# Kernel optimization log

Hardware: AMD Instinct MI355X
Metric: run time of the kernel (lower is better)

Reference implementation:

```python
import jax, jax.numpy as jnp
import numpy as np
from jax import lax

N, C, RC, H, W = 2, 256, 32, 64, 64  # RC = C // 8


def conv1x1(x, w, b):
    # x: [n,c,h,w], w: [o,c], b: [o]
    return jnp.einsum('nchw,oc->nohw', x, w) + b[None, :, None, None]


def conv3x3(x, w, b):
    # x: [n,c,h,w], w: [o,i,3,3]
    y = lax.conv_general_dilated(x, w, window_strides=(1, 1), padding='SAME',
                                 dimension_numbers=('NCHW', 'OIHW', 'NCHW'))
    return y + b[None, :, None, None]


def setup_inputs() -> dict:
    key = jax.random.key(0)
    ks = jax.random.split(key, 16)
    p = lambda k, s: jax.random.normal(k, s, dtype=jnp.float32) * 0.02
    z = lambda o: jnp.zeros((o,), jnp.float32)
    return {
        'rgb_feat': jax.random.normal(ks[0], (N, C, H, W), jnp.float32),
        'chm_feat': jax.random.normal(ks[1], (N, C, H, W), jnp.float32),
        'rgb_q_w': p(ks[2], (RC, C)), 'rgb_q_b': z(RC),
        'rgb_k_w': p(ks[3], (RC, C)), 'rgb_k_b': z(RC),
        'rgb_v_w': p(ks[4], (C, C)), 'rgb_v_b': z(C),
        'depth_q_w': p(ks[5], (RC, C)), 'depth_q_b': z(RC),
        'depth_k_w': p(ks[6], (RC, C)), 'depth_k_b': z(RC),
        'depth_v_w': p(ks[7], (C, C)), 'depth_v_b': z(C),
        'gate_w': p(ks[8], (C, 2 * C)), 'gate_b': z(C),
        'fus1_w': p(ks[9], (2 * C, 2 * C)), 'fus1_b': z(2 * C),
        'fus2_w': p(ks[10], (2 * C, 2 * C, 3, 3)), 'fus2_b': z(2 * C),
        'fus3_w': p(ks[11], (C, 2 * C)), 'fus3_b': z(C),
        'skip_w': p(ks[12], (C, 2 * C)), 'skip_b': z(C),
    }


def reference(rgb_feat, chm_feat,
              rgb_q_w, rgb_q_b, rgb_k_w, rgb_k_b, rgb_v_w, rgb_v_b,
              depth_q_w, depth_q_b, depth_k_w, depth_k_b, depth_v_w, depth_v_b,
              gate_w, gate_b, fus1_w, fus1_b, fus2_w, fus2_b,
              fus3_w, fus3_b, skip_w, skip_b):
    n, c, h, w = rgb_feat.shape
    hw = h * w
    flat = lambda t: t.reshape(n, t.shape[1], hw)

    rq = flat(conv1x1(rgb_feat, rgb_q_w, rgb_q_b))       # [n,rc,hw]
    rk = flat(conv1x1(rgb_feat, rgb_k_w, rgb_k_b))       # [n,rc,hw]
    rv = flat(conv1x1(rgb_feat, rgb_v_w, rgb_v_b))       # [n,c,hw]
    dq = flat(conv1x1(chm_feat, depth_q_w, depth_q_b))   # [n,rc,hw]
    dk = flat(conv1x1(chm_feat, depth_k_w, depth_k_b))   # [n,rc,hw]
    dv = flat(conv1x1(chm_feat, depth_v_w, depth_v_b))   # [n,c,hw]

    # rgb branch attended with depth-derived attention
    rgb_attn = jax.nn.softmax(jnp.einsum('nri,nrj->nij', dq, dk), axis=-1)  # [n,hw,hw]
    br = jnp.einsum('nci,nij->ncj', rv, rgb_attn).reshape(rgb_feat.shape) + rgb_feat

    # depth branch attended with rgb-derived attention
    depth_attn = jax.nn.softmax(jnp.einsum('nri,nrj->nij', rq, rk), axis=-1)
    bd = jnp.einsum('nci,nij->ncj', dv, depth_attn).reshape(chm_feat.shape) + chm_feat

    cat = jnp.concatenate([br, bd], axis=1)              # [n,2c,h,w]
    g = jax.nn.sigmoid(conv1x1(cat, gate_w, gate_b))     # [n,c,h,w]
    c_fused = br * g + bd * (1.0 - g)
    d_fused = br * bd
    f = jnp.concatenate([c_fused, d_fused], axis=1)      # [n,2c,h,w]

    y = jax.nn.relu(conv1x1(f, fus1_w, fus1_b))
    y = jax.nn.relu(conv3x3(y, fus2_w, fus2_b))
    y = conv1x1(y, fus3_w, fus3_b)
    fused = y + conv1x1(f, skip_w, skip_b)
    return fused
```

## Files before the change

### kernel.cpp

```cpp
#include <hip/hip_runtime.h>
#include <stdint.h>


typedef __bf16 bf16_t;
typedef __bf16 bf16x8 __attribute__((ext_vector_type(8)));
typedef float f32x4 __attribute__((ext_vector_type(4)));

#define HW 4096
#define NB 2

__device__ inline f32x4 mfma_bf16(bf16x8 a, bf16x8 b, f32x4 c) {
    return __builtin_amdgcn_mfma_f32_16x16x32_bf16(a, b, c, 0, 0, 0);
}

#define MAXJOB 12
struct CvtJobs {
    const float* src[MAXJOB];
    bf16_t* dst[MAXJOB];
    int vend[MAXJOB];
    int rowlen[MAXJOB];
    int rowstride[MAXJOB];
    int rowoff[MAXJOB];
};

__global__ __launch_bounds__(256) void convert_batch_k(CvtJobs J, int totalvec) {
    int gv = blockIdx.x * 256 + threadIdx.x;
    if (gv >= totalvec) return;
    int j = 0;
    while (gv >= J.vend[j]) j++;
    int vbase = (j == 0) ? 0 : J.vend[j - 1];
    int e = (gv - vbase) * 8;
    const float* s = J.src[j] + e;
    float4 f0 = *(const float4*)s;
    float4 f1 = *(const float4*)(s + 4);
    bf16x8 o;
    o[0] = (bf16_t)f0.x; o[1] = (bf16_t)f0.y; o[2] = (bf16_t)f0.z; o[3] = (bf16_t)f0.w;
    o[4] = (bf16_t)f1.x; o[5] = (bf16_t)f1.y; o[6] = (bf16_t)f1.z; o[7] = (bf16_t)f1.w;
    int di = e;
    if (J.rowlen[j])
        di = (e / J.rowlen[j]) * J.rowstride[j] + J.rowoff[j] + (e % J.rowlen[j]);
    *(bf16x8*)(J.dst[j] + di) = o;
}

__global__ __launch_bounds__(256) void pack_bias_k(const float* qr, const float* kr,
                                                   const float* qd, const float* kd,
                                                   const float* sb, const float* fb,
                                                   float* BQK_R, float* BQK_D, float* BSUM) {
    int t = threadIdx.x;
    if (t < 32) {
        BQK_R[t] = qr[t]; BQK_R[32 + t] = kr[t];
        BQK_D[t] = qd[t]; BQK_D[32 + t] = kd[t];
    }
    BSUM[t] = sb[t] + fb[t];
}

__global__ __launch_bounds__(256) void reorder_fus2_k(const float* __restrict__ src,
                                                      bf16_t* __restrict__ dst) {
    int idx = blockIdx.x * 256 + threadIdx.x;
    if (idx >= 512 * 4608) return;
    int o = idx / 4608;
    int t = idx % 4608;
    int t9 = t / 512;
    int c  = t % 512;
    dst[idx] = (bf16_t)src[(size_t)o * 4608 + c * 9 + t9];
}

template <int EPI, bool OUT_BF16, int NW>
__global__ __launch_bounds__(NW * 64) void gemm_k(const bf16_t* __restrict__ A,
                                                  const bf16_t* __restrict__ A2,
                                                  const bf16_t* __restrict__ B,
                                                  const float* __restrict__ bias,
                                                  const float* __restrict__ bias2,
                                                  void* __restrict__ outp,
                                                  const void* __restrict__ aux,
                                                  int M, int K, size_t strideB, size_t strideO) {
    __shared__ bf16_t Bt[64][72];
    const int t = threadIdx.x;
    const int mb = blockIdx.x, jb = blockIdx.y, n = blockIdx.z;
    const int w = t >> 6, lane = t & 63, quad = lane >> 4, l16 = lane & 15;
    const int MBLK = NW * 16;

    const bf16_t* Au = (n >= 2) ? A2 : A;
    const float* biasu = (n >= 2) ? bias2 : bias;

    const bf16_t* Bb = B + (size_t)n * strideB + jb * 64;

    f32x4 zero = {0.f, 0.f, 0.f, 0.f};
    f32x4 acc[4] = {zero, zero, zero, zero};

    const bf16_t* Arow = Au + (size_t)(mb * MBLK + w * 16 + l16) * K + quad * 8;

    for (int k0 = 0; k0 < K; k0 += 64) {
        if constexpr (NW == 4) {
            const bf16_t* src = Bb + (size_t)(k0 + lane) * HW + w * 16;
            bf16x8 v0 = *(const bf16x8*)src;
            bf16x8 v1 = *(const bf16x8*)(src + 8);
            __syncthreads();
#pragma unroll
            for (int e = 0; e < 8; e++) Bt[w * 16 + e][lane] = v0[e];
#pragma unroll
            for (int e = 0; e < 8; e++) Bt[w * 16 + 8 + e][lane] = v1[e];
        } else {
            const bf16_t* src = Bb + (size_t)(k0 + lane) * HW + w * 8;
            bf16x8 v0 = *(const bf16x8*)src;
            __syncthreads();
#pragma unroll
            for (int e = 0; e < 8; e++) Bt[w * 8 + e][lane] = v0[e];
        }
        __syncthreads();

        bf16x8 a0 = *(const bf16x8*)(Arow + k0);
        bf16x8 a1 = *(const bf16x8*)(Arow + k0 + 32);
#pragma unroll
        for (int ns = 0; ns < 4; ns++) {
            bf16x8 b0 = *(const bf16x8*)&Bt[ns * 16 + l16][quad * 8];
            bf16x8 b1 = *(const bf16x8*)&Bt[ns * 16 + l16][32 + quad * 8];
            acc[ns] = mfma_bf16(a0, b0, acc[ns]);
            acc[ns] = mfma_bf16(a1, b1, acc[ns]);
        }
    }

    if (EPI == 6) {
        const float scl = (w < 2) ? 1.44269504f : 1.0f;
#pragma unroll
        for (int ns = 0; ns < 4; ns++) {
            int col = jb * 64 + ns * 16 + l16;
            union { bf16_t h[4]; unsigned long long u; } pk;
#pragma unroll
            for (int rr = 0; rr < 4; rr++) {
                int m = w * 16 + quad * 4 + rr;
                pk.h[rr] = (bf16_t)((acc[ns][rr] + biasu[m]) * scl);
            }
            *(unsigned long long*)((bf16_t*)outp +
                ((size_t)n * HW + col) * 64 + w * 16 + quad * 4) = pk.u;
        }
    } else if (EPI == 7) {
        const int m_base = mb * MBLK + w * 16 + quad * 4;
#pragma unroll
        for (int ns = 0; ns < 4; ns++) {
            int col = jb * 64 + ns * 16 + l16;
            union { bf16_t h[4]; unsigned long long u; } pk;
#pragma unroll
            for (int rr = 0; rr < 4; rr++) {
                float v = acc[ns][rr] + biasu[m_base + rr];
                pk.h[rr] = (bf16_t)(v > 0.f ? v : 0.f);
            }
            *(unsigned long long*)((bf16_t*)outp +
                ((size_t)n * HW + col) * 512 + m_base) = pk.u;
        }
    } else if (EPI == 5) {
        const bf16_t* catp = (const bf16_t*)aux;
        bf16_t* f = (bf16_t*)outp;
#pragma unroll
        for (int ns = 0; ns < 4; ns++) {
#pragma unroll
            for (int rr = 0; rr < 4; rr++) {
                int m = mb * MBLK + w * 16 + quad * 4 + rr;
                int col = jb * 64 + ns * 16 + l16;
                float v = acc[ns][rr] + biasu[m];
                float g = 1.f / (1.f + __expf(-v));
                size_t base = (size_t)n * 512 * HW + (size_t)m * HW + col;
                float br = (float)catp[base];
                float bd = (float)catp[base + (size_t)256 * HW];
                size_t ob = (size_t)n * 1024 * HW + (size_t)m * HW + col;
                f[ob] = (bf16_t)(br * g + bd * (1.f - g));
                f[ob + (size_t)256 * HW] = (bf16_t)(br * bd);
            }
        }
    } else {
#pragma unroll
        for (int ns = 0; ns < 4; ns++) {
#pragma unroll
            for (int rr = 0; rr < 4; rr++) {
                int m = mb * MBLK + w * 16 + quad * 4 + rr;
                int col = jb * 64 + ns * 16 + l16;
                float v = acc[ns][rr] + biasu[m];
                if (EPI == 1) v = v > 0.f ? v : 0.f;
                size_t oi = (size_t)n * strideO + (size_t)m * HW + col;
                if (OUT_BF16) ((bf16_t*)outp)[oi] = (bf16_t)v;
                else ((float*)outp)[oi] = v;
            }
        }
    }
}

__global__ __launch_bounds__(256) void conv3_k(const bf16_t* __restrict__ A,
                                               const bf16_t* __restrict__ Y1n,
                                               const float* __restrict__ bias,
                                               bf16_t* __restrict__ outp,
                                               size_t strideN) {
    __shared__ bf16_t kTn[198][72];
    const int t = threadIdx.x;
    const int lin = blockIdx.x;
    const int n = lin & 1, mb = (lin >> 1) & 3, y = lin >> 3;
    const int w = t >> 6, lane = t & 63, quad = lane >> 4, l16 = lane & 15;

    f32x4 zero = {0.f, 0.f, 0.f, 0.f};
    f32x4 acc[2][4];
#pragma unroll
    for (int i = 0; i < 2; i++)
#pragma unroll
        for (int j = 0; j < 4; j++) acc[i][j] = zero;

    const bf16_t* Yb = Y1n + (size_t)n * HW * 512;

    const bf16_t* Arow0 = A + (size_t)(mb * 128 + w * 32 + l16) * 4608 + quad * 8;
    const bf16_t* Arow1 = Arow0 + (size_t)16 * 4608;

    int pxs[7], seg[7], gidx[7];
    bool ok[7], act[7];
#pragma unroll
    for (int i = 0; i < 7; i++) {
        int slot = t + i * 256;
        act[i] = slot < 1584;
        int ps = act[i] ? (slot >> 3) : 0;
        pxs[i] = ps;
        seg[i] = slot & 7;
        int r = ps / 66, xm = ps % 66;
        int yy = y + r - 1, xx = xm - 1;
        ok[i] = act[i] && ((unsigned)yy < 64u) && ((unsigned)xx < 64u);
        gidx[i] = ok[i] ? (yy * 64 + xx) : 0;
    }

    for (int c0 = 0; c0 < 512; c0 += 64) {
        bf16x8 vals[7];
#pragma unroll
        for (int i = 0; i < 7; i++) {
            bf16x8 v;
            if (ok[i]) {
                v = *(const bf16x8*)(Yb + (size_t)gidx[i] * 512 + c0 + seg[i] * 8);
            } else {
#pragma unroll
                for (int e = 0; e < 8; e++) v[e] = (bf16_t)0.f;
            }
            vals[i] = v;
        }
        __syncthreads();
#pragma unroll
        for (int i = 0; i < 7; i++)
            if (act[i]) *(bf16x8*)&kTn[pxs[i]][seg[i] * 8] = vals[i];
        __syncthreads();

#pragma unroll
        for (int t9 = 0; t9 < 9; t9++) {
            const int dy = t9 / 3, dx = t9 % 3;
            const bf16_t* ap0 = Arow0 + t9 * 512 + c0;
            const bf16_t* ap1 = Arow1 + t9 * 512 + c0;
            bf16x8 a00 = *(const bf16x8*)(ap0);
            bf16x8 a01 = *(const bf16x8*)(ap0 + 32);
            bf16x8 a10 = *(const bf16x8*)(ap1);
            bf16x8 a11 = *(const bf16x8*)(ap1 + 32);
#pragma unroll
            for (int ns = 0; ns < 4; ns++) {
                int p = dy * 66 + ns * 16 + l16 + dx;
                bf16x8 b0 = *(const bf16x8*)&kTn[p][quad * 8];
                bf16x8 b1 = *(const bf16x8*)&kTn[p][32 + quad * 8];
                acc[0][ns] = mfma_bf16(a00, b0, acc[0][ns]);
                acc[0][ns] = mfma_bf16(a01, b1, acc[0][ns]);
                acc[1][ns] = mfma_bf16(a10, b0, acc[1][ns]);
                acc[1][ns] = mfma_bf16(a11, b1, acc[1][ns]);
            }
        }
    }

#pragma unroll
    for (int ms = 0; ms < 2; ms++) {
#pragma unroll
        for (int ns = 0; ns < 4; ns++) {
#pragma unroll
            for (int rr = 0; rr < 4; rr++) {
                int m = mb * 128 + w * 32 + ms * 16 + quad * 4 + rr;
                int x = ns * 16 + l16;
                float v = acc[ms][ns][rr] + bias[m];
                v = v > 0.f ? v : 0.f;
                outp[(size_t)n * strideN + (size_t)m * HW + y * 64 + x] = (bf16_t)v;
            }
        }
    }
}

#define ASTEP(P, ASC, AVC, ASN, AVN, ITN)                                      \
    {                                                                          \
        _Pragma("unroll")                                                      \
        for (int ns = 0; ns < 4; ns++) {                                       \
            f32x4 s = mfma_bf16(ASC, bS[ns], zero);                            \
            union { bf16_t h[4]; unsigned long long u; } pk;                   \
            float zs = 0.f;                                                    \
            _Pragma("unroll")                                                  \
            for (int rr = 0; rr < 4; rr++) {                                   \
                pk.h[rr] = (bf16_t)__builtin_amdgcn_exp2f(s[rr]);              \
                zs += (float)pk.h[rr];                                         \
            }                                                                  \
            zacc[ns] += zs;                                                    \
            *(unsigned long long*)&PT[P][ns * 16 + l16][w * 16 + quad * 4] = pk.u; \
        }                                                                      \
        ASN = *(const bf16x8*)(Qa + (size_t)((ITN) & 63) * (64 * 64));         \
        AVN[0][0] = *(const bf16x8*)(Vr0 + ((ITN) & 63) * 64);                 \
        AVN[0][1] = *(const bf16x8*)(Vr0 + ((ITN) & 63) * 64 + 32);            \
        AVN[1][0] = *(const bf16x8*)(Vr1 + ((ITN) & 63) * 64);                 \
        AVN[1][1] = *(const bf16x8*)(Vr1 + ((ITN) & 63) * 64 + 32);            \
        asm volatile("s_waitcnt lgkmcnt(0)" ::: "memory");                     \
        __builtin_amdgcn_s_barrier();                                          \
        __builtin_amdgcn_sched_barrier(0);                                     \
        __builtin_amdgcn_s_setprio(1);                                         \
        _Pragma("unroll")                                                      \
        for (int ns = 0; ns < 4; ns++) {                                       \
            bf16x8 b0 = *(const bf16x8*)&PT[P][ns * 16 + l16][quad * 8];       \
            bf16x8 b1 = *(const bf16x8*)&PT[P][ns * 16 + l16][32 + quad * 8];  \
            _Pragma("unroll")                                                  \
            for (int ct = 0; ct < 2; ct++) {                                   \
                acc[ct][ns] = mfma_bf16(AVC[ct][0], b0, acc[ct][ns]);          \
                acc[ct][ns] = mfma_bf16(AVC[ct][1], b1, acc[ct][ns]);          \
            }                                                                  \
        }                                                                      \
        __builtin_amdgcn_s_setprio(0);                                         \
    }

__global__ __launch_bounds__(256) void attn3_k(const bf16_t* __restrict__ QKT,
                                               const bf16_t* __restrict__ V,
                                               const float* __restrict__ rgb_feat,
                                               const float* __restrict__ chm_feat,
                                               bf16_t* __restrict__ CAT) {
    __shared__ bf16_t PT[2][64][72];
    __shared__ float Zp[4][64];
    const int t = threadIdx.x;
    const int lin = blockIdx.x;
    const int cb = lin & 1, z = (lin >> 1) & 3, jb = lin >> 3;
    const int w = t >> 6, lane = t & 63, quad = lane >> 4, l16 = lane & 15;
    const int qs = z ^ 2, n = z & 1;

    const bf16_t* Q = QKT + (size_t)qs * HW * 64;

    bf16x8 bS[4];
#pragma unroll
    for (int ns = 0; ns < 4; ns++)
        bS[ns] = *(const bf16x8*)(Q + (size_t)(jb * 64 + ns * 16 + l16) * 64 + 32 + quad * 8);

    f32x4 zero = {0.f, 0.f, 0.f, 0.f};
    f32x4 acc[2][4];
#pragma unroll
    for (int i = 0; i < 2; i++)
#pragma unroll
        for (int j = 0; j < 4; j++) acc[i][j] = zero;
    float zacc[4] = {0.f, 0.f, 0.f, 0.f};

    const bf16_t* Vr0 = V + ((size_t)z * 256 + cb * 128 + w * 16 + l16) * HW + quad * 8;
    const bf16_t* Vr1 = Vr0 + (size_t)64 * HW;
    const bf16_t* Qa = Q + (size_t)(w * 16 + l16) * 64 + quad * 8;

    bf16x8 aSa, aSb, aVa[2][2], aVb[2][2];
    aSa = *(const bf16x8*)Qa;
    aVa[0][0] = *(const bf16x8*)(Vr0);
    aVa[0][1] = *(const bf16x8*)(Vr0 + 32);
    aVa[1][0] = *(const bf16x8*)(Vr1);
    aVa[1][1] = *(const bf16x8*)(Vr1 + 32);

    for (int ii = 0; ii < 32; ii++) {
        ASTEP(0, aSa, aVa, aSb, aVb, 2 * ii + 1);
        ASTEP(1, aSb, aVb, aSa, aVa, 2 * ii + 2);
    }

#pragma unroll
    for (int ns = 0; ns < 4; ns++) {
        zacc[ns] += __shfl_xor(zacc[ns], 16, 64);
        zacc[ns] += __shfl_xor(zacc[ns], 32, 64);
    }
    if (lane < 16) {
#pragma unroll
        for (int ns = 0; ns < 4; ns++) Zp[w][ns * 16 + lane] = zacc[ns];
    }
    __syncthreads();
    float rz[4];
#pragma unroll
    for (int ns = 0; ns < 4; ns++) {
        float ssum = 0.f;
#pragma unroll
        for (int ww = 0; ww < 4; ww++) ssum += Zp[ww][ns * 16 + l16];
        rz[ns] = 1.f / ssum;
    }

    const float* feat = ((z < 2) ? rgb_feat : chm_feat) + (size_t)n * 256 * HW;
    bf16_t* outp = CAT + (size_t)n * 512 * HW + (size_t)(z < 2 ? 0 : 256) * HW;
#pragma unroll
    for (int ct = 0; ct < 2; ct++) {
#pragma unroll
        for (int ns = 0; ns < 4; ns++) {
#pragma unroll
            for (int rr = 0; rr < 4; rr++) {
                int c = cb * 128 + ct * 64 + w * 16 + quad * 4 + rr;
                int col = jb * 64 + ns * 16 + l16;
                float v = acc[ct][ns][rr] * rz[ns] + feat[(size_t)c * HW + col];
                outp[(size_t)c * HW + col] = (bf16_t)v;
            }
        }
    }
}

extern "C" void kernel_launch(void* const* d_in, const int* in_sizes, int n_in,
                              void* d_out, int out_size, void* d_ws, size_t ws_size,
                              hipStream_t stream) {
    (void)in_sizes; (void)n_in; (void)out_size; (void)ws_size;

    const float* rgb_feat  = (const float*)d_in[0];
    const float* chm_feat  = (const float*)d_in[1];
    const float* rgb_q_w   = (const float*)d_in[2];
    const float* rgb_q_b   = (const float*)d_in[3];
    const float* rgb_k_w   = (const float*)d_in[4];
    const float* rgb_k_b   = (const float*)d_in[5];
    const float* rgb_v_w   = (const float*)d_in[6];
    const float* rgb_v_b   = (const float*)d_in[7];
    const float* depth_q_w = (const float*)d_in[8];
    const float* depth_q_b = (const float*)d_in[9];
    const float* depth_k_w = (const float*)d_in[10];
    const float* depth_k_b = (const float*)d_in[11];
    const float* depth_v_w = (const float*)d_in[12];
    const float* depth_v_b = (const float*)d_in[13];
    const float* gate_w    = (const float*)d_in[14];
    const float* gate_b    = (const float*)d_in[15];
    const float* fus1_w    = (const float*)d_in[16];
    const float* fus1_b    = (const float*)d_in[17];
    const float* fus2_w    = (const float*)d_in[18];
    const float* fus2_b    = (const float*)d_in[19];
    const float* fus3_w    = (const float*)d_in[20];
    const float* fus3_b    = (const float*)d_in[21];
    const float* skip_w    = (const float*)d_in[22];
    const float* skip_b    = (const float*)d_in[23];

    char* ws = (char*)d_ws;
    size_t off = 0;
    auto alloc = [&](size_t bytes) -> char* {
        char* p = ws + off;
        off += (bytes + 255) & ~(size_t)255;
        return p;
    };

    bf16_t* WQK_R = (bf16_t*)alloc(64 * 256 * 2);
    bf16_t* WQK_D = (bf16_t*)alloc(64 * 256 * 2);
    bf16_t* WV_R  = (bf16_t*)alloc(256 * 256 * 2);
    bf16_t* WV_D  = (bf16_t*)alloc(256 * 256 * 2);
    bf16_t* WGATE = (bf16_t*)alloc(256 * 512 * 2);
    bf16_t* WFUS1 = (bf16_t*)alloc(512 * 512 * 2);
    bf16_t* WFUS2 = (bf16_t*)alloc(512 * 4608 * 2);
    bf16_t* WCAT  = (bf16_t*)alloc(256 * 1024 * 2);
    float*  BQK_R = (float*)alloc(64 * 4);
    float*  BQK_D = (float*)alloc(64 * 4);
    float*  BSUM  = (float*)alloc(256 * 4);
    bf16_t* XB    = (bf16_t*)alloc((size_t)4 * 256 * HW * 2);
    bf16_t* QKT   = (bf16_t*)alloc((size_t)4 * HW * 64 * 2);
    bf16_t* V4    = (bf16_t*)alloc((size_t)4 * 256 * HW * 2);
    bf16_t* CAT   = (bf16_t*)alloc((size_t)NB * 512 * HW * 2);
    bf16_t* FY    = (bf16_t*)alloc((size_t)NB * 1024 * HW * 2);
    bf16_t* Y1    = (bf16_t*)alloc((size_t)NB * HW * 512 * 2);

    bf16_t* XR = XB;
    bf16_t* XC = XB + (size_t)2 * 256 * HW;

    CvtJobs J;
    int cum = 0, nj = 0;
    auto addjob = [&](const float* s, bf16_t* d, int cnt, int rl, int rs, int ro) {
        J.src[nj] = s; J.dst[nj] = d; cum += cnt / 8; J.vend[nj] = cum;
        J.rowlen[nj] = rl; J.rowstride[nj] = rs; J.rowoff[nj] = ro; nj++;
    };
    addjob(rgb_feat, XR, NB * 256 * HW, 0, 0, 0);
    addjob(chm_feat, XC, NB * 256 * HW, 0, 0, 0);
    addjob(rgb_q_w, WQK_R, 32 * 256, 0, 0, 0);
    addjob(rgb_k_w, WQK_R + 32 * 256, 32 * 256, 0, 0, 0);
    addjob(depth_q_w, WQK_D, 32 * 256, 0, 0, 0);
    addjob(depth_k_w, WQK_D + 32 * 256, 32 * 256, 0, 0, 0);
    addjob(rgb_v_w, WV_R, 256 * 256, 0, 0, 0);
    addjob(depth_v_w, WV_D, 256 * 256, 0, 0, 0);
    addjob(gate_w, WGATE, 256 * 512, 0, 0, 0);
    addjob(fus1_w, WFUS1, 512 * 512, 0, 0, 0);
    addjob(skip_w, WCAT, 256 * 512, 512, 1024, 0);
    addjob(fus3_w, WCAT, 256 * 512, 512, 1024, 512);
    int totalvec = cum;
    convert_batch_k<<<dim3((totalvec + 255) / 256), 256, 0, stream>>>(J, totalvec);
    reorder_fus2_k<<<dim3(512 * 4608 / 256), 256, 0, stream>>>(fus2_w, WFUS2);
    pack_bias_k<<<dim3(1), 256, 0, stream>>>(rgb_q_b, rgb_k_b, depth_q_b, depth_k_b,
                                             skip_b, fus3_b, BQK_R, BQK_D, BSUM);

    gemm_k<6, true, 4><<<dim3(1, 64, 4), 256, 0, stream>>>(
        WQK_R, WQK_D, XB, BQK_R, BQK_D, QKT, nullptr, 64, 256, (size_t)256 * HW, 0);

    gemm_k<0, true, 8><<<dim3(2, 64, 4), 512, 0, stream>>>(
        WV_R, WV_D, XB, rgb_v_b, depth_v_b, V4, nullptr, 256, 256, (size_t)256 * HW, (size_t)256 * HW);

    attn3_k<<<dim3(512), 256, 0, stream>>>(QKT, V4, rgb_feat, chm_feat, CAT);

    gemm_k<5, true, 8><<<dim3(2, 64, NB), 512, 0, stream>>>(
        WGATE, WGATE, CAT, gate_b, gate_b, FY, CAT, 256, 512, (size_t)512 * HW, 0);

    gemm_k<7, true, 8><<<dim3(4, 64, NB), 512, 0, stream>>>(
        WFUS1, WFUS1, FY, fus1_b, fus1_b, Y1, nullptr, 512, 512, (size_t)1024 * HW, 0);

    conv3_k<<<dim3(512), 256, 0, stream>>>(WFUS2, Y1, fus2_b,
                                           FY + (size_t)512 * HW, (size_t)1024 * HW);

    gemm_k<0, false, 8><<<dim3(2, 64, NB), 512, 0, stream>>>(
        WCAT, WCAT, FY, BSUM, BSUM, d_out, nullptr, 256, 1024, (size_t)1024 * HW, (size_t)256 * HW);
}
```

Before: 339.2 us.

## Merge prep kernels, fuse QK and V projections, prefetch global tiles across barriers

Folds the three setup kernels (convert, fus2 reorder, bias pack) into one launch, and merges the QK and V projection GEMMs into a single kernel with 640 blocks. The GEMM and conv3 main loops now issue the next K-chunk's global load before the MFMAs and store it to LDS after the barrier, which is software prefetching. A custom barrier waits only on LDS counters so those in-flight global loads are not drained. This cuts launch overhead and hides load latency, at the cost of extra registers and a wasted wrap-around prefetch on the last iteration.

```diff
diff --git a/kernel.cpp b/kernel.cpp
--- a/kernel.cpp
+++ b/kernel.cpp
@@ -12,6 +12,13 @@
 __device__ inline f32x4 mfma_bf16(bf16x8 a, bf16x8 b, f32x4 c) {
     return __builtin_amdgcn_mfma_f32_16x16x32_bf16(a, b, c, 0, 0, 0);
 }
+
+#define LBAR()                                                                 \
+    do {                                                                       \
+        asm volatile("s_waitcnt lgkmcnt(0)" ::: "memory");                     \
+        __builtin_amdgcn_s_barrier();                                          \
+        __builtin_amdgcn_sched_barrier(0);                                     \
+    } while (0)
 
 #define MAXJOB 12
 struct CvtJobs {
@@ -23,62 +30,163 @@
     int rowoff[MAXJOB];
 };
 
-__global__ __launch_bounds__(256) void convert_batch_k(CvtJobs J, int totalvec) {
-    int gv = blockIdx.x * 256 + threadIdx.x;
-    if (gv >= totalvec) return;
-    int j = 0;
-    while (gv >= J.vend[j]) j++;
-    int vbase = (j == 0) ? 0 : J.vend[j - 1];
-    int e = (gv - vbase) * 8;
-    const float* s = J.src[j] + e;
-    float4 f0 = *(const float4*)s;
-    float4 f1 = *(const float4*)(s + 4);
-    bf16x8 o;
-    o[0] = (bf16_t)f0.x; o[1] = (bf16_t)f0.y; o[2] = (bf16_t)f0.z; o[3] = (bf16_t)f0.w;
-    o[4] = (bf16_t)f1.x; o[5] = (bf16_t)f1.y; o[6] = (bf16_t)f1.z; o[7] = (bf16_t)f1.w;
-    int di = e;
-    if (J.rowlen[j])
-        di = (e / J.rowlen[j]) * J.rowstride[j] + J.rowoff[j] + (e % J.rowlen[j]);
-    *(bf16x8*)(J.dst[j] + di) = o;
-}
-
-__global__ __launch_bounds__(256) void pack_bias_k(const float* qr, const float* kr,
-                                                   const float* qd, const float* kd,
-                                                   const float* sb, const float* fb,
-                                                   float* BQK_R, float* BQK_D, float* BSUM) {
-    int t = threadIdx.x;
-    if (t < 32) {
-        BQK_R[t] = qr[t]; BQK_R[32 + t] = kr[t];
-        BQK_D[t] = qd[t]; BQK_D[32 + t] = kd[t];
-    }
-    BSUM[t] = sb[t] + fb[t];
-}
-
-__global__ __launch_bounds__(256) void reorder_fus2_k(const float* __restrict__ src,
-                                                      bf16_t* __restrict__ dst) {
-    int idx = blockIdx.x * 256 + threadIdx.x;
-    if (idx >= 512 * 4608) return;
-    int o = idx / 4608;
-    int t = idx % 4608;
-    int t9 = t / 512;
-    int c  = t % 512;
-    dst[idx] = (bf16_t)src[(size_t)o * 4608 + c * 9 + t9];
-}
-
-template <int EPI, bool OUT_BF16, int NW>
-__global__ __launch_bounds__(NW * 64) void gemm_k(const bf16_t* __restrict__ A,
-                                                  const bf16_t* __restrict__ A2,
-                                                  const bf16_t* __restrict__ B,
-                                                  const float* __restrict__ bias,
-                                                  const float* __restrict__ bias2,
-                                                  void* __restrict__ outp,
-                                                  const void* __restrict__ aux,
-                                                  int M, int K, size_t strideB, size_t strideO) {
+__global__ __launch_bounds__(256) void prep_k(CvtJobs J, int totalvec, int cvtBlocks,
+                                              const float* __restrict__ fus2_src,
+                                              bf16_t* __restrict__ fus2_dst,
+                                              const float* qr, const float* kr,
+                                              const float* qd, const float* kd,
+                                              const float* sb, const float* fb,
+                                              float* BQK_R, float* BQK_D, float* BSUM) {
+    const int b = blockIdx.x, t = threadIdx.x;
+    if (b < cvtBlocks) {
+        int gv = b * 256 + t;
+        if (gv >= totalvec) return;
+        int j = 0;
+        while (gv >= J.vend[j]) j++;
+        int vbase = (j == 0) ? 0 : J.vend[j - 1];
+        int e = (gv - vbase) * 8;
+        const float* s = J.src[j] + e;
+        float4 f0 = *(const float4*)s;
+        float4 f1 = *(const float4*)(s + 4);
+        bf16x8 o;
+        o[0] = (bf16_t)f0.x; o[1] = (bf16_t)f0.y; o[2] = (bf16_t)f0.z; o[3] = (bf16_t)f0.w;
+        o[4] = (bf16_t)f1.x; o[5] = (bf16_t)f1.y; o[6] = (bf16_t)f1.z; o[7] = (bf16_t)f1.w;
+        int di = e;
+        if (J.rowlen[j])
+            di = (e / J.rowlen[j]) * J.rowstride[j] + J.rowoff[j] + (e % J.rowlen[j]);
+        *(bf16x8*)(J.dst[j] + di) = o;
+    } else if (b < cvtBlocks + 9216) {
+        int idx = (b - cvtBlocks) * 256 + t;
+        int o = idx / 4608;
+        int tt = idx % 4608;
+        int t9 = tt / 512;
+        int c  = tt % 512;
+        fus2_dst[idx] = (bf16_t)fus2_src[(size_t)o * 4608 + c * 9 + t9];
+    } else {
+        if (t < 32) {
+            BQK_R[t] = qr[t]; BQK_R[32 + t] = kr[t];
+            BQK_D[t] = qd[t]; BQK_D[32 + t] = kd[t];
+        }
+        BSUM[t] = sb[t] + fb[t];
+    }
+}
+
+__global__ __launch_bounds__(512) void proj_k(const bf16_t* __restrict__ WV_R,
+                                              const bf16_t* __restrict__ WV_D,
+                                              const bf16_t* __restrict__ WQK_R,
+                                              const bf16_t* __restrict__ WQK_D,
+                                              const bf16_t* __restrict__ XB,
+                                              const float* __restrict__ vb_r,
+                                              const float* __restrict__ vb_d,
+                                              const float* __restrict__ bqk_r,
+                                              const float* __restrict__ bqk_d,
+                                              bf16_t* __restrict__ V4,
+                                              bf16_t* __restrict__ QKT) {
+    __shared__ bf16_t Bt[2][64][72];
+    const int t = threadIdx.x, b = blockIdx.x;
+    const int w = t >> 6, lane = t & 63, quad = lane >> 4, l16 = lane & 15;
+
+    f32x4 zero = {0.f, 0.f, 0.f, 0.f};
+    f32x4 acc[4] = {zero, zero, zero, zero};
+
+    if (b < 512) {
+        const int mb = b & 1, jb = (b >> 1) & 63, n = b >> 7;
+        const bf16_t* Au = (n >= 2) ? WV_D : WV_R;
+        const float* biasu = (n >= 2) ? vb_d : vb_r;
+        const bf16_t* Bb = XB + (size_t)n * (256 * HW) + jb * 64;
+        const bf16_t* Arow = Au + (size_t)(mb * 128 + w * 16 + l16) * 256 + quad * 8;
+
+        bf16x8 v0 = *(const bf16x8*)(Bb + (size_t)lane * HW + w * 8);
+        for (int k0 = 0; k0 < 256; k0 += 64) {
+            LBAR();
+#pragma unroll
+            for (int e = 0; e < 8; e++) Bt[0][w * 8 + e][lane] = v0[e];
+            LBAR();
+            const int kn = (k0 + 64 < 256) ? k0 + 64 : 0;
+            bf16x8 vp = *(const bf16x8*)(Bb + (size_t)(kn + lane) * HW + w * 8);
+            bf16x8 a0 = *(const bf16x8*)(Arow + k0);
+            bf16x8 a1 = *(const bf16x8*)(Arow + k0 + 32);
+#pragma unroll
+            for (int ns = 0; ns < 4; ns++) {
+                bf16x8 b0 = *(const bf16x8*)&Bt[0][ns * 16 + l16][quad * 8];
+                bf16x8 b1 = *(const bf16x8*)&Bt[0][ns * 16 + l16][32 + quad * 8];
+                acc[ns] = mfma_bf16(a0, b0, acc[ns]);
+                acc[ns] = mfma_bf16(a1, b1, acc[ns]);
+            }
+            v0 = vp;
+        }
+#pragma unroll
+        for (int ns = 0; ns < 4; ns++) {
+#pragma unroll
+            for (int rr = 0; rr < 4; rr++) {
+                int m = mb * 128 + w * 16 + quad * 4 + rr;
+                int col = jb * 64 + ns * 16 + l16;
+                V4[(size_t)n * 256 * HW + (size_t)m * HW + col] =
+                    (bf16_t)(acc[ns][rr] + biasu[m]);
+            }
+        }
+    } else {
+        const int qb = b - 512;
+        const int n2 = qb >> 5, jpair = qb & 31;
+        const int g = w >> 2, wg = w & 3;
+        const int jb = jpair * 2 + g;
+        const bf16_t* Au = (n2 >= 2) ? WQK_D : WQK_R;
+        const float* biasu = (n2 >= 2) ? bqk_d : bqk_r;
+        const bf16_t* Bb = XB + (size_t)n2 * (256 * HW) + jb * 64;
+        const bf16_t* Arow = Au + (size_t)(wg * 16 + l16) * 256 + quad * 8;
+
+        bf16x8 v0 = *(const bf16x8*)(Bb + (size_t)lane * HW + wg * 16);
+        bf16x8 v1 = *(const bf16x8*)(Bb + (size_t)lane * HW + wg * 16 + 8);
+        for (int k0 = 0; k0 < 256; k0 += 64) {
+            LBAR();
+#pragma unroll
+            for (int e = 0; e < 8; e++) Bt[g][wg * 16 + e][lane] = v0[e];
+#pragma unroll
+            for (int e = 0; e < 8; e++) Bt[g][wg * 16 + 8 + e][lane] = v1[e];
+            LBAR();
+            const int kn = (k0 + 64 < 256) ? k0 + 64 : 0;
+            bf16x8 p0 = *(const bf16x8*)(Bb + (size_t)(kn + lane) * HW + wg * 16);
+            bf16x8 p1 = *(const bf16x8*)(Bb + (size_t)(kn + lane) * HW + wg * 16 + 8);
+            bf16x8 a0 = *(const bf16x8*)(Arow + k0);
+            bf16x8 a1 = *(const bf16x8*)(Arow + k0 + 32);
+#pragma unroll
+            for (int ns = 0; ns < 4; ns++) {
+                bf16x8 b0 = *(const bf16x8*)&Bt[g][ns * 16 + l16][quad * 8];
+                bf16x8 b1 = *(const bf16x8*)&Bt[g][ns * 16 + l16][32 + quad * 8];
+                acc[ns] = mfma_bf16(a0, b0, acc[ns]);
+                acc[ns] = mfma_bf16(a1, b1, acc[ns]);
+            }
+            v0 = p0; v1 = p1;
+        }
+        const float scl = (wg < 2) ? 1.44269504f : 1.0f;
+#pragma unroll
+        for (int ns = 0; ns < 4; ns++) {
+            int col = jb * 64 + ns * 16 + l16;
+            union { bf16_t h[4]; unsigned long long u; } pk;
+#pragma unroll
+            for (int rr = 0; rr < 4; rr++) {
+                int m = wg * 16 + quad * 4 + rr;
+                pk.h[rr] = (bf16_t)((acc[ns][rr] + biasu[m]) * scl);
+            }
+            *(unsigned long long*)(QKT +
+                ((size_t)n2 * HW + col) * 64 + wg * 16 + quad * 4) = pk.u;
+        }
+    }
+}
+
+template <int EPI, bool OUT_BF16>
+__global__ __launch_bounds__(512) void gemm_k(const bf16_t* __restrict__ A,
+                                              const bf16_t* __restrict__ A2,
+                                              const bf16_t* __restrict__ B,
+                                              const float* __restrict__ bias,
+                                              const float* __restrict__ bias2,
+                                              void* __restrict__ outp,
+                                              const void* __restrict__ aux,
+                                              int M, int K, size_t strideB, size_t strideO) {
     __shared__ bf16_t Bt[64][72];
     const int t = threadIdx.x;
     const int mb = blockIdx.x, jb = blockIdx.y, n = blockIdx.z;
     const int w = t >> 6, lane = t & 63, quad = lane >> 4, l16 = lane & 15;
-    const int MBLK = NW * 16;
 
     const bf16_t* Au = (n >= 2) ? A2 : A;
     const float* biasu = (n >= 2) ? bias2 : bias;
@@ -88,27 +196,16 @@
     f32x4 zero = {0.f, 0.f, 0.f, 0.f};
     f32x4 acc[4] = {zero, zero, zero, zero};
 
-    const bf16_t* Arow = Au + (size_t)(mb * MBLK + w * 16 + l16) * K + quad * 8;
-
+    const bf16_t* Arow = Au + (size_t)(mb * 128 + w * 16 + l16) * K + quad * 8;
+
+    bf16x8 v0 = *(const bf16x8*)(Bb + (size_t)lane * HW + w * 8);
     for (int k0 = 0; k0 < K; k0 += 64) {
-        if constexpr (NW == 4) {
-            const bf16_t* src = Bb + (size_t)(k0 + lane) * HW + w * 16;
-            bf16x8 v0 = *(const bf16x8*)src;
-            bf16x8 v1 = *(const bf16x8*)(src + 8);
-            __syncthreads();
-#pragma unroll
-            for (int e = 0; e < 8; e++) Bt[w * 16 + e][lane] = v0[e];
-#pragma unroll
-            for (int e = 0; e < 8; e++) Bt[w * 16 + 8 + e][lane] = v1[e];
-        } else {
-            const bf16_t* src = Bb + (size_t)(k0 + lane) * HW + w * 8;
-            bf16x8 v0 = *(const bf16x8*)src;
-            __syncthreads();
-#pragma unroll
-            for (int e = 0; e < 8; e++) Bt[w * 8 + e][lane] = v0[e];
-        }
-        __syncthreads();
-
+        LBAR();
+#pragma unroll
+        for (int e = 0; e < 8; e++) Bt[w * 8 + e][lane] = v0[e];
+        LBAR();
+        const int kn = (k0 + 64 < K) ? k0 + 64 : 0;
+        bf16x8 vp = *(const bf16x8*)(Bb + (size_t)(kn + lane) * HW + w * 8);
         bf16x8 a0 = *(const bf16x8*)(Arow + k0);
         bf16x8 a1 = *(const bf16x8*)(Arow + k0 + 32);
 #pragma unroll
@@ -118,24 +215,11 @@
             acc[ns] = mfma_bf16(a0, b0, acc[ns]);
             acc[ns] = mfma_bf16(a1, b1, acc[ns]);
         }
-    }
-
-    if (EPI == 6) {
-        const float scl = (w < 2) ? 1.44269504f : 1.0f;
-#pragma unroll
-        for (int ns = 0; ns < 4; ns++) {
-            int col = jb * 64 + ns * 16 + l16;
-            union { bf16_t h[4]; unsigned long long u; } pk;
-#pragma unroll
-            for (int rr = 0; rr < 4; rr++) {
-                int m = w * 16 + quad * 4 + rr;
-                pk.h[rr] = (bf16_t)((acc[ns][rr] + biasu[m]) * scl);
-            }
-            *(unsigned long long*)((bf16_t*)outp +
-                ((size_t)n * HW + col) * 64 + w * 16 + quad * 4) = pk.u;
-        }
-    } else if (EPI == 7) {
-        const int m_base = mb * MBLK + w * 16 + quad * 4;
+        v0 = vp;
+    }
+
+    if (EPI == 7) {
+        const int m_base = mb * 128 + w * 16 + quad * 4;
 #pragma unroll
         for (int ns = 0; ns < 4; ns++) {
             int col = jb * 64 + ns * 16 + l16;
@@ -155,7 +239,7 @@
         for (int ns = 0; ns < 4; ns++) {
 #pragma unroll
             for (int rr = 0; rr < 4; rr++) {
-                int m = mb * MBLK + w * 16 + quad * 4 + rr;
+                int m = mb * 128 + w * 16 + quad * 4 + rr;
                 int col = jb * 64 + ns * 16 + l16;
                 float v = acc[ns][rr] + biasu[m];
                 float g = 1.f / (1.f + __expf(-v));
@@ -172,10 +256,9 @@
         for (int ns = 0; ns < 4; ns++) {
 #pragma unroll
             for (int rr = 0; rr < 4; rr++) {
-                int m = mb * MBLK + w * 16 + quad * 4 + rr;
+                int m = mb * 128 + w * 16 + quad * 4 + rr;
                 int col = jb * 64 + ns * 16 + l16;
                 float v = acc[ns][rr] + biasu[m];
-                if (EPI == 1) v = v > 0.f ? v : 0.f;
                 size_t oi = (size_t)n * strideO + (size_t)m * HW + col;
                 if (OUT_BF16) ((bf16_t*)outp)[oi] = (bf16_t)v;
                 else ((float*)outp)[oi] = v;
@@ -222,24 +305,38 @@
         gidx[i] = ok[i] ? (yy * 64 + xx) : 0;
     }
 
+    bf16x8 vals[7];
+#pragma unroll
+    for (int i = 0; i < 7; i++) {
+        bf16x8 v;
+        if (ok[i]) {
+            v = *(const bf16x8*)(Yb + (size_t)gidx[i] * 512 + seg[i] * 8);
+        } else {
+#pragma unroll
+            for (int e = 0; e < 8; e++) v[e] = (bf16_t)0.f;
+        }
+        vals[i] = v;
+    }
+
     for (int c0 = 0; c0 < 512; c0 += 64) {
-        bf16x8 vals[7];
+        LBAR();
+#pragma unroll
+        for (int i = 0; i < 7; i++)
+            if (act[i]) *(bf16x8*)&kTn[pxs[i]][seg[i] * 8] = vals[i];
+        LBAR();
+
+        const int cn = (c0 + 64) & 511;
 #pragma unroll
         for (int i = 0; i < 7; i++) {
             bf16x8 v;
             if (ok[i]) {
-                v = *(const bf16x8*)(Yb + (size_t)gidx[i] * 512 + c0 + seg[i] * 8);
+                v = *(const bf16x8*)(Yb + (size_t)gidx[i] * 512 + cn + seg[i] * 8);
             } else {
 #pragma unroll
                 for (int e = 0; e < 8; e++) v[e] = (bf16_t)0.f;
             }
             vals[i] = v;
         }
-        __syncthreads();
-#pragma unroll
-        for (int i = 0; i < 7; i++)
-            if (act[i]) *(bf16x8*)&kTn[pxs[i]][seg[i] * 8] = vals[i];
-        __syncthreads();
 
 #pragma unroll
         for (int t9 = 0; t9 < 9; t9++) {
@@ -474,28 +571,27 @@
     addjob(skip_w, WCAT, 256 * 512, 512, 1024, 0);
     addjob(fus3_w, WCAT, 256 * 512, 512, 1024, 512);
     int totalvec = cum;
-    convert_batch_k<<<dim3((totalvec + 255) / 256), 256, 0, stream>>>(J, totalvec);
-    reorder_fus2_k<<<dim3(512 * 4608 / 256), 256, 0, stream>>>(fus2_w, WFUS2);
-    pack_bias_k<<<dim3(1), 256, 0, stream>>>(rgb_q_b, rgb_k_b, depth_q_b, depth_k_b,
-                                             skip_b, fus3_b, BQK_R, BQK_D, BSUM);
-
-    gemm_k<6, true, 4><<<dim3(1, 64, 4), 256, 0, stream>>>(
-        WQK_R, WQK_D, XB, BQK_R, BQK_D, QKT, nullptr, 64, 256, (size_t)256 * HW, 0);
-
-    gemm_k<0, true, 8><<<dim3(2, 64, 4), 512, 0, stream>>>(
-        WV_R, WV_D, XB, rgb_v_b, depth_v_b, V4, nullptr, 256, 256, (size_t)256 * HW, (size_t)256 * HW);
+    int cvtBlocks = (totalvec + 255) / 256;
+    int prepBlocks = cvtBlocks + 9216 + 1;
+    prep_k<<<dim3(prepBlocks), 256, 0, stream>>>(
+        J, totalvec, cvtBlocks, fus2_w, WFUS2,
+        rgb_q_b, rgb_k_b, depth_q_b, depth_k_b, skip_b, fus3_b,
+        BQK_R, BQK_D, BSUM);
+
+    proj_k<<<dim3(640), 512, 0, stream>>>(
+        WV_R, WV_D, WQK_R, WQK_D, XB, rgb_v_b, depth_v_b, BQK_R, BQK_D, V4, QKT);
 
     attn3_k<<<dim3(512), 256, 0, stream>>>(QKT, V4, rgb_feat, chm_feat, CAT);
 
-    gemm_k<5, true, 8><<<dim3(2, 64, NB), 512, 0, stream>>>(
+    gemm_k<5, true><<<dim3(2, 64, NB), 512, 0, stream>>>(
         WGATE, WGATE, CAT, gate_b, gate_b, FY, CAT, 256, 512, (size_t)512 * HW, 0);
 
-    gemm_k<7, true, 8><<<dim3(4, 64, NB), 512, 0, stream>>>(
+    gemm_k<7, true><<<dim3(4, 64, NB), 512, 0, stream>>>(
         WFUS1, WFUS1, FY, fus1_b, fus1_b, Y1, nullptr, 512, 512, (size_t)1024 * HW, 0);
 
     conv3_k<<<dim3(512), 256, 0, stream>>>(WFUS2, Y1, fus2_b,
                                            FY + (size_t)512 * HW, (size_t)1024 * HW);
 
-    gemm_k<0, false, 8><<<dim3(2, 64, NB), 512, 0, stream>>>(
+    gemm_k<0, false><<<dim3(2, 64, NB), 512, 0, stream>>>(
         WCAT, WCAT, FY, BSUM, BSUM, d_out, nullptr, 256, 1024, (size_t)1024 * HW, (size_t)256 * HW);
 }
```

Measured after the change: 335.6 us. Within noise of the previous version (-1.0%).
